# Kernel optimization log

Measured on AMD Instinct MI355X. Metric: run time of the kernel, lower is better.

## Reference

```python
import jax, jax.numpy as jnp
import numpy as np

B, H, S, D = 4, 16, 2048, 64
TEMPERATURE = 8.0  # sqrt(d_k)
NEG_INF = -1e9


def setup_inputs() -> dict:
    key = jax.random.key(0)
    kq, kk, kv, kb = jax.random.split(key, 4)
    q = jax.random.normal(kq, (B, H, S, D), dtype=jnp.float32)
    k = jax.random.normal(kk, (B, H, S, D), dtype=jnp.float32)
    v = jax.random.normal(kv, (B, H, S, D), dtype=jnp.float32)
    mask = jnp.ones((B, 1, S, S), dtype=jnp.int32)
    attn_bias = jax.random.normal(kb, (B, H, S, S), dtype=jnp.float32)
    return {"q": q, "k": k, "v": v, "mask": mask, "attn_bias": attn_bias}


def reference(q, k, v, mask, attn_bias):
    # scores: [B,H,S,S]
    attn = jnp.einsum("bhqd,bhkd->bhqk", q / TEMPERATURE, k)
    attn = jnp.where(mask == 0, NEG_INF, attn)
    attn = attn + attn_bias
    # dropout p=0.0 -> identity
    norm_attn = jax.nn.softmax(attn, axis=-1)
    output = jnp.einsum("bhqk,bhkd->bhqd", norm_attn, v)
    return (output, attn)
```

## Files before the change

kernel.cpp:

```cpp
#include <hip/hip_runtime.h>
#include <math.h>

#define NBATCH 4
#define NHEAD  16
#define SEQ    2048
#define HDIM   64
#define QT     64
#define KT     64
#define NTILE  (SEQ / KT)
#define PSHIFT 8.0f

using f4v = __attribute__((ext_vector_type(4))) float;
using i4v = __attribute__((ext_vector_type(4))) int;
using h4  = __attribute__((ext_vector_type(4))) _Float16;
using h8  = __attribute__((ext_vector_type(8))) _Float16;

__device__ __forceinline__ void lds_barrier() {
    asm volatile("s_waitcnt lgkmcnt(0)" ::: "memory");
    __builtin_amdgcn_s_barrier();
}

__global__ __launch_bounds__(256) void cvt_k(const float* __restrict__ in,
                                             _Float16* __restrict__ out) {
    size_t i = ((size_t)blockIdx.x * 256 + threadIdx.x) * 8;
    f4v a = *reinterpret_cast<const f4v*>(in + i);
    f4v b = *reinterpret_cast<const f4v*>(in + i + 4);
    h8 o = { (_Float16)a[0], (_Float16)a[1], (_Float16)a[2], (_Float16)a[3],
             (_Float16)b[0], (_Float16)b[1], (_Float16)b[2], (_Float16)b[3] };
    *reinterpret_cast<h8*>(out + i) = o;
}

__global__ __launch_bounds__(256) void xpose_v(const float* __restrict__ vin,
                                               _Float16* __restrict__ vout) {
    __shared__ _Float16 vls[256][72];
    const int t  = threadIdx.x;
    const int c  = blockIdx.x;
    const int bh = blockIdx.y;
    const float* src = vin + ((size_t)bh * SEQ + (size_t)c * 256) * HDIM;
    #pragma unroll
    for (int it = 0; it < 16; ++it) {
        int i   = t + it * 256;
        int key = i >> 4;
        int d4  = (i & 15) << 2;
        f4v x = *reinterpret_cast<const f4v*>(src + (size_t)key * HDIM + d4);
        h4 hx = { (_Float16)x[0], (_Float16)x[1], (_Float16)x[2], (_Float16)x[3] };
        *reinterpret_cast<h4*>(&vls[key][d4]) = hx;
    }
    __syncthreads();
    _Float16* dst = vout + (size_t)bh * HDIM * SEQ + (size_t)c * 256;
    #pragma unroll
    for (int it = 0; it < 8; ++it) {
        int u  = t + it * 256;
        int d  = u >> 5;
        int k8 = (u & 31) << 3;
        h8 o;
        #pragma unroll
        for (int j = 0; j < 8; ++j) o[j] = vls[k8 + j][d];
        *reinterpret_cast<h8*>(dst + (size_t)d * SEQ + k8) = o;
    }
}

__global__ __launch_bounds__(256) void fused_attn_v18(
    const float* __restrict__ qp, const _Float16* __restrict__ kf16,
    const _Float16* __restrict__ vt16, const int* __restrict__ maskp,
    const float* __restrict__ biasp, float* __restrict__ outp,
    float* __restrict__ attnp)
{
    __shared__ _Float16 sT[64 * 68];
    __shared__ _Float16 psh[QT][72];
    __shared__ _Float16 ksh[2][KT * HDIM];
    __shared__ _Float16 vsT[2][HDIM * KT];

    const int t    = threadIdx.x;
    const int w    = t >> 6;
    const int lane = t & 63;
    const int g    = lane >> 4;
    const int r    = lane & 15;

    const int bh = blockIdx.y;
    const int b  = bh >> 4;
    const int q0 = blockIdx.x * QT;

    const int r0 = 16 * w + 4 * g;
    const int c0 = r << 2;

    const float*    qg    = qp    + ((size_t)bh * SEQ + q0) * HDIM;
    const _Float16* kg16  = kf16  + (size_t)bh * SEQ * HDIM;
    const _Float16* vtg   = vt16  + (size_t)bh * HDIM * SEQ;
    const float*    biasg = biasp + ((size_t)bh * SEQ + q0) * SEQ;
    const int*      maskg = maskp + ((size_t)b  * SEQ + q0) * SEQ;
    float*          attng = attnp + ((size_t)bh * SEQ + q0) * SEQ;
    float*          outg  = outp  + ((size_t)bh * SEQ + q0) * HDIM;

    h8 qf[2];
    {
        const float* p8 = qg + (16 * w + r) * HDIM;
        #pragma unroll
        for (int s = 0; s < 2; ++s) {
            f4v lo = *reinterpret_cast<const f4v*>(p8 + 32 * s + 8 * g);
            f4v hi = *reinterpret_cast<const f4v*>(p8 + 32 * s + 8 * g + 4);
            #pragma unroll
            for (int j = 0; j < 4; ++j) {
                qf[s][j]     = (_Float16)(0.125f * lo[j]);
                qf[s][j + 4] = (_Float16)(0.125f * hi[j]);
            }
        }
    }

    f4v  oacc[4];
    float l_i[4];
    #pragma unroll
    for (int i = 0; i < 4; ++i) { oacc[i] = (f4v){0.f,0.f,0.f,0.f}; l_i[i] = 0.f; }

    h8 kstg[2][2], vstg[2][2];

    auto issueKV = [&](int tt, int set) {
        const int k0 = tt * KT;
        #pragma unroll
        for (int u = 0; u < 2; ++u) {
            int i = t + (u << 8);
            int row = i >> 3, col8 = (i & 7) << 3;
            kstg[set][u] = *reinterpret_cast<const h8*>(kg16 + (size_t)(k0 + row) * HDIM + col8);
        }
        #pragma unroll
        for (int u = 0; u < 2; ++u) {
            int i = t + (u << 8);
            int d = i >> 3, k8 = (i & 7) << 3;
            vstg[set][u] = *reinterpret_cast<const h8*>(vtg + (size_t)d * SEQ + k0 + k8);
        }
    };

    auto write_stage = [&](int buf, int set) {
        #pragma unroll
        for (int u = 0; u < 2; ++u) {
            int i = t + (u << 8);
            int row = i >> 3, cb = (i & 7) << 4;
            char* dst = (char*)&ksh[buf][0] + row * 128 + (cb ^ ((row & 7) << 4));
            *reinterpret_cast<h8*>(dst) = kstg[set][u];
        }
        #pragma unroll
        for (int u = 0; u < 2; ++u) {
            int i = t + (u << 8);
            int d = i >> 3, cb = (i & 7) << 4;
            char* dst = (char*)&vsT[buf][0] + d * 128 + (cb ^ ((d & 7) << 4));
            *reinterpret_cast<h8*>(dst) = vstg[set][u];
        }
    };

    auto issue_bm = [&](int tt, f4v* bv, i4v* mv) {
        const int k0 = tt * KT;
        #pragma unroll
        for (int i = 0; i < 4; ++i) {
            size_t rowoff = (size_t)(r0 + i) * SEQ + k0 + c0;
            mv[i] = *reinterpret_cast<const i4v*>(maskg + rowoff);
            bv[i] = *reinterpret_cast<const f4v*>(biasg + rowoff);
        }
    };

    auto compute = [&](int tt, int buf, f4v* bvC, i4v* mvC) {
        const int k0 = tt * KT;
        f4v acc[4];
        #pragma unroll
        for (int tc = 0; tc < 4; ++tc) acc[tc] = (f4v){0.f,0.f,0.f,0.f};
        #pragma unroll
        for (int tc = 0; tc < 4; ++tc) {
            #pragma unroll
            for (int s = 0; s < 2; ++s) {
                const char* src = (const char*)&ksh[buf][0]
                    + (16 * tc + r) * 128 + ((64 * s + 16 * g) ^ ((r & 7) << 4));
                h8 kf = *reinterpret_cast<const h8*>(src);
                acc[tc] = __builtin_amdgcn_mfma_f32_16x16x32_f16(qf[s], kf, acc[tc], 0, 0, 0);
            }
        }
        #pragma unroll
        for (int tc = 0; tc < 4; ++tc) {
            h4 sh4 = { (_Float16)acc[tc][0], (_Float16)acc[tc][1],
                       (_Float16)acc[tc][2], (_Float16)acc[tc][3] };
            char* dst = (char*)sT + (16 * tc + r) * 136 + (32 * w + 8 * g);
            *reinterpret_cast<h4*>(dst) = sh4;
        }
        h4 sr[4];
        #pragma unroll
        for (int m = 0; m < 4; ++m) {
            const char* src = (const char*)sT + (4 * r + m) * 136 + (32 * w + 8 * g);
            sr[m] = *reinterpret_cast<const h4*>(src);
        }
        #pragma unroll
        for (int i = 0; i < 4; ++i) {
            size_t rowoff = (size_t)(r0 + i) * SEQ + k0 + c0;
            f4v sc;
            #pragma unroll
            for (int j = 0; j < 4; ++j)
                sc[j] = (mvC[i][j] == 0 ? -1e9f : (float)sr[j][i]) + bvC[i][j];
            *reinterpret_cast<f4v*>(attng + rowoff) = sc;
            f4v p;
            #pragma unroll
            for (int j = 0; j < 4; ++j) { p[j] = __expf(sc[j] - PSHIFT); l_i[i] += p[j]; }
            h4 ph = { (_Float16)p[0], (_Float16)p[1], (_Float16)p[2], (_Float16)p[3] };
            *reinterpret_cast<h4*>(&psh[r0 + i][c0]) = ph;
        }
        #pragma unroll
        for (int s = 0; s < 2; ++s) {
            h8 pf = *reinterpret_cast<const h8*>(&psh[16 * w + r][32 * s + 8 * g]);
            #pragma unroll
            for (int tc = 0; tc < 4; ++tc) {
                const char* src = (const char*)&vsT[buf][0]
                    + (16 * tc + r) * 128 + ((64 * s + 16 * g) ^ ((r & 7) << 4));
                h8 vf = *reinterpret_cast<const h8*>(src);
                oacc[tc] = __builtin_amdgcn_mfma_f32_16x16x32_f16(pf, vf, oacc[tc], 0, 0, 0);
            }
        }
    };

    f4v bA[4], bB[4]; i4v mA[4], mB[4];
    issueKV(0, 0);
    issueKV(1, 1);
    issue_bm(0, bA, mA);
    issue_bm(1, bB, mB);
    write_stage(0, 0);
    lds_barrier();

    for (int t2 = 0; t2 < NTILE; t2 += 2) {
        {
            const bool more = (t2 + 2 < NTILE);
            if (more) issueKV(t2 + 2, 0);
            compute(t2, 0, bA, mA);
            if (more) issue_bm(t2 + 2, bA, mA);
            write_stage(1, 1);
            lds_barrier();
        }
        {
            const bool more3 = (t2 + 3 < NTILE);
            const bool more2 = (t2 + 2 < NTILE);
            if (more3) issueKV(t2 + 3, 1);
            compute(t2 + 1, 1, bB, mB);
            if (more3) issue_bm(t2 + 3, bB, mB);
            if (more2) write_stage(0, 0);
            lds_barrier();
        }
    }

    #pragma unroll
    for (int i = 0; i < 4; ++i) {
        #pragma unroll
        for (int off = 1; off < 16; off <<= 1)
            l_i[i] += __shfl_xor(l_i[i], off);
    }
    #pragma unroll
    for (int jr = 0; jr < 4; ++jr) {
        float inv = 1.f / l_i[jr];
        #pragma unroll
        for (int tc = 0; tc < 4; ++tc)
            outg[(size_t)(r0 + jr) * HDIM + 16 * tc + r] = oacc[tc][jr] * inv;
    }
}

__global__ __launch_bounds__(256) void fused_attn_fb(
    const float* __restrict__ qp, const float* __restrict__ kp,
    const float* __restrict__ vp, const int* __restrict__ maskp,
    const float* __restrict__ biasp, float* __restrict__ outp,
    float* __restrict__ attnp)
{
    __shared__ _Float16 s_tile[QT][72];
    __shared__ _Float16 ksh[2][KT][72];
    __shared__ _Float16 vsT[2][HDIM][72];

    const int t    = threadIdx.x;
    const int w    = t >> 6;
    const int lane = t & 63;
    const int g    = lane >> 4;
    const int r    = lane & 15;
    const int bh = blockIdx.y;
    const int b  = bh >> 4;
    const int q0 = blockIdx.x * QT;
    const int r0 = 16 * w + 4 * g;
    const int c0 = r << 2;

    const float* qg    = qp    + ((size_t)bh * SEQ + q0) * HDIM;
    const float* kg    = kp    + (size_t)bh * SEQ * HDIM;
    const float* vg    = vp    + (size_t)bh * SEQ * HDIM;
    const float* biasg = biasp + ((size_t)bh * SEQ + q0) * SEQ;
    const int*   maskg = maskp + ((size_t)b  * SEQ + q0) * SEQ;
    float*       attng = attnp + ((size_t)bh * SEQ + q0) * SEQ;
    float*       outg  = outp  + ((size_t)bh * SEQ + q0) * HDIM;

    h8 qf[2];
    {
        const float* p8 = qg + (16 * w + r) * HDIM;
        #pragma unroll
        for (int s = 0; s < 2; ++s) {
            f4v lo = *reinterpret_cast<const f4v*>(p8 + 32 * s + 8 * g);
            f4v hi = *reinterpret_cast<const f4v*>(p8 + 32 * s + 8 * g + 4);
            #pragma unroll
            for (int j = 0; j < 4; ++j) {
                qf[s][j]     = (_Float16)(0.125f * lo[j]);
                qf[s][j + 4] = (_Float16)(0.125f * hi[j]);
            }
        }
    }
    f4v  oacc[4]; float l_i[4];
    #pragma unroll
    for (int i = 0; i < 4; ++i) { oacc[i] = (f4v){0.f,0.f,0.f,0.f}; l_i[i] = 0.f; }
    f4v kreg[4]; float vreg[16];

    auto issue_loads = [&](int tt) {
        const int k0 = tt * KT;
        #pragma unroll
        for (int it = 0; it < 4; ++it) {
            int i = t + (it << 8);
            int key = i >> 4, c4 = (i & 15) << 2;
            kreg[it] = *reinterpret_cast<const f4v*>(kg + (size_t)(k0 + key) * HDIM + c4);
        }
        #pragma unroll
        for (int it = 0; it < 4; ++it) {
            int kb = 4 * it + w;
            #pragma unroll
            for (int j = 0; j < 4; ++j)
                vreg[4 * it + j] = vg[(size_t)(k0 + 4 * kb + j) * HDIM + lane];
        }
    };
    auto write_stage = [&](int buf) {
        #pragma unroll
        for (int it = 0; it < 4; ++it) {
            int i = t + (it << 8);
            int key = i >> 4, c4 = (i & 15) << 2;
            h4 kh = { (_Float16)kreg[it][0], (_Float16)kreg[it][1],
                      (_Float16)kreg[it][2], (_Float16)kreg[it][3] };
            *reinterpret_cast<h4*>(&ksh[buf][key][c4]) = kh;
        }
        #pragma unroll
        for (int it = 0; it < 4; ++it) {
            int kb = 4 * it + w;
            h4 vh = { (_Float16)vreg[4*it+0], (_Float16)vreg[4*it+1],
                      (_Float16)vreg[4*it+2], (_Float16)vreg[4*it+3] };
            *reinterpret_cast<h4*>(&vsT[buf][lane][4 * kb]) = vh;
        }
    };
    auto issue_bm = [&](int tt, f4v* bv, i4v* mv) {
        const int k0 = tt * KT;
        #pragma unroll
        for (int i = 0; i < 4; ++i) {
            size_t rowoff = (size_t)(r0 + i) * SEQ + k0 + c0;
            mv[i] = *reinterpret_cast<const i4v*>(maskg + rowoff);
            bv[i] = *reinterpret_cast<const f4v*>(biasg + rowoff);
        }
    };
    auto compute = [&](int tt, int buf, f4v* bvC, i4v* mvC) {
        const int k0 = tt * KT;
        f4v acc[4];
        #pragma unroll
        for (int tc = 0; tc < 4; ++tc) acc[tc] = (f4v){0.f,0.f,0.f,0.f};
        #pragma unroll
        for (int tc = 0; tc < 4; ++tc) {
            #pragma unroll
            for (int s = 0; s < 2; ++s) {
                h8 kf = *reinterpret_cast<const h8*>(&ksh[buf][16 * tc + r][32 * s + 8 * g]);
                acc[tc] = __builtin_amdgcn_mfma_f32_16x16x32_f16(qf[s], kf, acc[tc], 0, 0, 0);
            }
        }
        #pragma unroll
        for (int tc = 0; tc < 4; ++tc) {
            #pragma unroll
            for (int j = 0; j < 4; ++j)
                s_tile[r0 + j][16 * tc + r] = (_Float16)acc[tc][j];
        }
        #pragma unroll
        for (int i = 0; i < 4; ++i) {
            size_t rowoff = (size_t)(r0 + i) * SEQ + k0 + c0;
            h4 sh = *reinterpret_cast<const h4*>(&s_tile[r0 + i][c0]);
            f4v sc;
            #pragma unroll
            for (int j = 0; j < 4; ++j)
                sc[j] = (mvC[i][j] == 0 ? -1e9f : (float)sh[j]) + bvC[i][j];
            *reinterpret_cast<f4v*>(attng + rowoff) = sc;
            f4v p;
            #pragma unroll
            for (int j = 0; j < 4; ++j) { p[j] = __expf(sc[j] - PSHIFT); l_i[i] += p[j]; }
            h4 ph = { (_Float16)p[0], (_Float16)p[1], (_Float16)p[2], (_Float16)p[3] };
            *reinterpret_cast<h4*>(&s_tile[r0 + i][c0]) = ph;
        }
        #pragma unroll
        for (int s = 0; s < 2; ++s) {
            h8 pf = *reinterpret_cast<const h8*>(&s_tile[16 * w + r][32 * s + 8 * g]);
            #pragma unroll
            for (int tc = 0; tc < 4; ++tc) {
                h8 vf = *reinterpret_cast<const h8*>(&vsT[buf][16 * tc + r][32 * s + 8 * g]);
                oacc[tc] = __builtin_amdgcn_mfma_f32_16x16x32_f16(pf, vf, oacc[tc], 0, 0, 0);
            }
        }
    };

    f4v bA[4], bB[4]; i4v mA[4], mB[4];
    issue_loads(0); issue_bm(0, bA, mA); write_stage(0); lds_barrier();
    for (int t2 = 0; t2 < NTILE; t2 += 2) {
        {
            issue_loads(t2 + 1); issue_bm(t2 + 1, bB, mB);
            compute(t2, 0, bA, mA);
            write_stage(1); lds_barrier();
        }
        {
            const bool more = (t2 + 2 < NTILE);
            if (more) { issue_loads(t2 + 2); issue_bm(t2 + 2, bA, mA); }
            compute(t2 + 1, 1, bB, mB);
            if (more) write_stage(0);
            lds_barrier();
        }
    }
    #pragma unroll
    for (int i = 0; i < 4; ++i) {
        #pragma unroll
        for (int off = 1; off < 16; off <<= 1)
            l_i[i] += __shfl_xor(l_i[i], off);
    }
    #pragma unroll
    for (int jr = 0; jr < 4; ++jr) {
        float inv = 1.f / l_i[jr];
        #pragma unroll
        for (int tc = 0; tc < 4; ++tc)
            outg[(size_t)(r0 + jr) * HDIM + 16 * tc + r] = oacc[tc][jr] * inv;
    }
}

extern "C" void kernel_launch(void* const* d_in, const int* in_sizes, int n_in,
                              void* d_out, int out_size, void* d_ws, size_t ws_size,
                              hipStream_t stream) {
    const float* q    = (const float*)d_in[0];
    const float* k    = (const float*)d_in[1];
    const float* v    = (const float*)d_in[2];
    const int*   mask = (const int*)  d_in[3];
    const float* bias = (const float*)d_in[4];
    float* out  = (float*)d_out;
    float* attn = out + (size_t)NBATCH * NHEAD * SEQ * HDIM;

    dim3 grid(SEQ / QT, NBATCH * NHEAD);
    const size_t kvbytes = (size_t)NBATCH * NHEAD * SEQ * HDIM * sizeof(_Float16);
    if (ws_size >= 2 * kvbytes) {
        _Float16* kf16 = (_Float16*)d_ws;
        _Float16* vt16 = (_Float16*)((char*)d_ws + kvbytes);
        cvt_k<<<dim3(4096), dim3(256), 0, stream>>>(k, kf16);
        xpose_v<<<dim3(8, NBATCH * NHEAD), dim3(256), 0, stream>>>(v, vt16);
        fused_attn_v18<<<grid, dim3(256), 0, stream>>>(q, kf16, vt16, mask, bias, out, attn);
    } else {
        fused_attn_fb<<<grid, dim3(256), 0, stream>>>(q, k, v, mask, bias, out, attn);
    }
}
```

Measured before the change: 550.1 us.

## Load K/V MFMA operands directly from global memory, dropping LDS staging

Removes the double-buffered shared-memory staging of the fp16 K and transposed V tiles, along with the block-wide barriers. Each wave now fetches its MFMA operands straight from global memory, relying on L2/L1 caching. The mask tile is packed into a 16-bit register bitmask to cut register use. The aim is to drop barrier stalls and LDS traffic and raise occupancy. The cost is that all four waves load every K/V tile separately, which adds cache traffic in a kernel already dominated by streaming bias reads and score writes.

```diff
diff --git a/kernel.cpp b/kernel.cpp
--- a/kernel.cpp
+++ b/kernel.cpp
@@ -60,7 +60,7 @@
     }
 }
 
-__global__ __launch_bounds__(256) void fused_attn_v18(
+__global__ __launch_bounds__(256) void fused_attn_v19(
     const float* __restrict__ qp, const _Float16* __restrict__ kf16,
     const _Float16* __restrict__ vt16, const int* __restrict__ maskp,
     const float* __restrict__ biasp, float* __restrict__ outp,
@@ -68,8 +68,6 @@
 {
     __shared__ _Float16 sT[64 * 68];
     __shared__ _Float16 psh[QT][72];
-    __shared__ _Float16 ksh[2][KT * HDIM];
-    __shared__ _Float16 vsT[2][HDIM * KT];
 
     const int t    = threadIdx.x;
     const int w    = t >> 6;
@@ -112,52 +110,22 @@
     #pragma unroll
     for (int i = 0; i < 4; ++i) { oacc[i] = (f4v){0.f,0.f,0.f,0.f}; l_i[i] = 0.f; }
 
-    h8 kstg[2][2], vstg[2][2];
-
-    auto issueKV = [&](int tt, int set) {
-        const int k0 = tt * KT;
-        #pragma unroll
-        for (int u = 0; u < 2; ++u) {
-            int i = t + (u << 8);
-            int row = i >> 3, col8 = (i & 7) << 3;
-            kstg[set][u] = *reinterpret_cast<const h8*>(kg16 + (size_t)(k0 + row) * HDIM + col8);
-        }
-        #pragma unroll
-        for (int u = 0; u < 2; ++u) {
-            int i = t + (u << 8);
-            int d = i >> 3, k8 = (i & 7) << 3;
-            vstg[set][u] = *reinterpret_cast<const h8*>(vtg + (size_t)d * SEQ + k0 + k8);
-        }
-    };
-
-    auto write_stage = [&](int buf, int set) {
-        #pragma unroll
-        for (int u = 0; u < 2; ++u) {
-            int i = t + (u << 8);
-            int row = i >> 3, cb = (i & 7) << 4;
-            char* dst = (char*)&ksh[buf][0] + row * 128 + (cb ^ ((row & 7) << 4));
-            *reinterpret_cast<h8*>(dst) = kstg[set][u];
-        }
-        #pragma unroll
-        for (int u = 0; u < 2; ++u) {
-            int i = t + (u << 8);
-            int d = i >> 3, cb = (i & 7) << 4;
-            char* dst = (char*)&vsT[buf][0] + d * 128 + (cb ^ ((d & 7) << 4));
-            *reinterpret_cast<h8*>(dst) = vstg[set][u];
-        }
-    };
-
-    auto issue_bm = [&](int tt, f4v* bv, i4v* mv) {
-        const int k0 = tt * KT;
+    auto issue_bm = [&](int tt, f4v* bv, unsigned& mbits) {
+        const int k0 = tt * KT;
+        unsigned mb = 0;
         #pragma unroll
         for (int i = 0; i < 4; ++i) {
             size_t rowoff = (size_t)(r0 + i) * SEQ + k0 + c0;
-            mv[i] = *reinterpret_cast<const i4v*>(maskg + rowoff);
-            bv[i] = *reinterpret_cast<const f4v*>(biasg + rowoff);
-        }
-    };
-
-    auto compute = [&](int tt, int buf, f4v* bvC, i4v* mvC) {
+            i4v mm = *reinterpret_cast<const i4v*>(maskg + rowoff);
+            bv[i]  = *reinterpret_cast<const f4v*>(biasg + rowoff);
+            #pragma unroll
+            for (int j = 0; j < 4; ++j)
+                mb |= (mm[j] != 0 ? 1u : 0u) << (4 * i + j);
+        }
+        mbits = mb;
+    };
+
+    auto compute = [&](int tt, f4v* bvC, unsigned mbC) {
         const int k0 = tt * KT;
         f4v acc[4];
         #pragma unroll
@@ -166,9 +134,8 @@
         for (int tc = 0; tc < 4; ++tc) {
             #pragma unroll
             for (int s = 0; s < 2; ++s) {
-                const char* src = (const char*)&ksh[buf][0]
-                    + (16 * tc + r) * 128 + ((64 * s + 16 * g) ^ ((r & 7) << 4));
-                h8 kf = *reinterpret_cast<const h8*>(src);
+                h8 kf = *reinterpret_cast<const h8*>(
+                    kg16 + (size_t)(k0 + 16 * tc + r) * HDIM + 32 * s + 8 * g);
                 acc[tc] = __builtin_amdgcn_mfma_f32_16x16x32_f16(qf[s], kf, acc[tc], 0, 0, 0);
             }
         }
@@ -191,7 +158,7 @@
             f4v sc;
             #pragma unroll
             for (int j = 0; j < 4; ++j)
-                sc[j] = (mvC[i][j] == 0 ? -1e9f : (float)sr[j][i]) + bvC[i][j];
+                sc[j] = (((mbC >> (4 * i + j)) & 1) ? (float)sr[j][i] : -1e9f) + bvC[i][j];
             *reinterpret_cast<f4v*>(attng + rowoff) = sc;
             f4v p;
             #pragma unroll
@@ -204,40 +171,20 @@
             h8 pf = *reinterpret_cast<const h8*>(&psh[16 * w + r][32 * s + 8 * g]);
             #pragma unroll
             for (int tc = 0; tc < 4; ++tc) {
-                const char* src = (const char*)&vsT[buf][0]
-                    + (16 * tc + r) * 128 + ((64 * s + 16 * g) ^ ((r & 7) << 4));
-                h8 vf = *reinterpret_cast<const h8*>(src);
+                h8 vf = *reinterpret_cast<const h8*>(
+                    vtg + (size_t)(16 * tc + r) * SEQ + k0 + 32 * s + 8 * g);
                 oacc[tc] = __builtin_amdgcn_mfma_f32_16x16x32_f16(pf, vf, oacc[tc], 0, 0, 0);
             }
         }
     };
 
-    f4v bA[4], bB[4]; i4v mA[4], mB[4];
-    issueKV(0, 0);
-    issueKV(1, 1);
+    f4v bA[4], bB[4]; unsigned mA, mB;
     issue_bm(0, bA, mA);
-    issue_bm(1, bB, mB);
-    write_stage(0, 0);
-    lds_barrier();
-
     for (int t2 = 0; t2 < NTILE; t2 += 2) {
-        {
-            const bool more = (t2 + 2 < NTILE);
-            if (more) issueKV(t2 + 2, 0);
-            compute(t2, 0, bA, mA);
-            if (more) issue_bm(t2 + 2, bA, mA);
-            write_stage(1, 1);
-            lds_barrier();
-        }
-        {
-            const bool more3 = (t2 + 3 < NTILE);
-            const bool more2 = (t2 + 2 < NTILE);
-            if (more3) issueKV(t2 + 3, 1);
-            compute(t2 + 1, 1, bB, mB);
-            if (more3) issue_bm(t2 + 3, bB, mB);
-            if (more2) write_stage(0, 0);
-            lds_barrier();
-        }
+        issue_bm(t2 + 1, bB, mB);
+        compute(t2, bA, mA);
+        if (t2 + 2 < NTILE) issue_bm(t2 + 2, bA, mA);
+        compute(t2 + 1, bB, mB);
     }
 
     #pragma unroll
@@ -439,7 +386,7 @@
         _Float16* vt16 = (_Float16*)((char*)d_ws + kvbytes);
         cvt_k<<<dim3(4096), dim3(256), 0, stream>>>(k, kf16);
         xpose_v<<<dim3(8, NBATCH * NHEAD), dim3(256), 0, stream>>>(v, vt16);
-        fused_attn_v18<<<grid, dim3(256), 0, stream>>>(q, kf16, vt16, mask, bias, out, attn);
+        fused_attn_v19<<<grid, dim3(256), 0, stream>>>(q, kf16, vt16, mask, bias, out, attn);
     } else {
         fused_attn_fb<<<grid, dim3(256), 0, stream>>>(q, k, v, mask, bias, out, attn);
     }
```

After: 820.2 us. 1.49x slower.
